# Optimization experiments

Measured on AMD Instinct MI355X. Metric: run time of the kernel, lower is better.

Reference implementation:

```python
import jax, jax.numpy as jnp
import numpy as np

B, M, D, DE = 2, 256, 256, 64  # batch, tokens, in_dim, dep_embed_dim


def setup_inputs() -> dict:
    key = jax.random.key(0)
    ks = jax.random.split(key, 10)
    features = jax.random.normal(ks[0], (B, M + 1, D), jnp.float32)
    dep_type_adj = jax.random.normal(ks[1], (B, M, M, DE), jnp.float32)
    adj = (jax.random.uniform(ks[2], (B, M, M)) < 0.05).astype(jnp.int32)
    idx = jnp.arange(M)
    adj = adj.at[:, idx, idx].set(1)
    asp_start = jax.random.randint(ks[3], (B,), 0, 200, dtype=jnp.int32)
    asp_end = asp_start + 16
    s = lambda fan_in: 1.0 / np.sqrt(fan_in)
    Wz = jax.random.normal(ks[4], (D, D), jnp.float32) * s(D)
    bz = jax.random.normal(ks[5], (D,), jnp.float32) * s(D)
    Wa = jax.random.normal(ks[6], (D + DE + D,), jnp.float32) * s(D + DE + D)
    Wm = jax.random.normal(ks[7], (D, D + DE), jnp.float32) * s(D + DE)
    Wh = jax.random.normal(ks[8], (D, 2 * D), jnp.float32) * s(2 * D)
    return dict(features=features, dep_type_adj=dep_type_adj, deprel_adj=adj,
                asp_start=asp_start, asp_end=asp_end,
                Wz=Wz, bz=bz, Wa=Wa, Wm=Wm, Wh=Wh)


def reference(features, dep_type_adj, deprel_adj, asp_start, asp_end, Wz, bz, Wa, Wm, Wh):
    # z_linear
    zf = features @ Wz.T + bz                              # [B, M+1, D]
    f = zf[:, 1:]                                          # token feats [B, M, D]
    asp = zf[0, 1:]                                        # NOTE: original indexes features[0] (batch 0)

    # candidate neighbors for node i: out-edges (i,j) then in-edges (j,i) -> 2M slots
    dep_cat = jnp.concatenate([dep_type_adj, jnp.swapaxes(dep_type_adj, 1, 2)], axis=2)  # [B,M,2M,DE]
    mask = jnp.concatenate([deprel_adj, jnp.swapaxes(deprel_adj, 1, 2)], axis=2) != 0    # [B,M,2M]

    # attention_layer weight split over [dep | neighbor_feat | aspect_feat]
    wa_dep, wa_nf, wa_asp = Wa[:DE], Wa[DE:DE + D], Wa[DE + D:]
    s = (jnp.einsum('bike,e->bik', dep_cat, wa_dep)
         + jnp.tile(f @ wa_nf, (1, 2))[:, None, :]
         + (asp @ wa_asp)[None, :, None])                  # [B,M,2M]
    s = jnp.where(s > 0, s, 0.01 * s)                      # LeakyReLU(0.01)
    big_neg = jnp.finfo(s.dtype).min
    w = jax.nn.softmax(jnp.where(mask, s, big_neg), axis=-1)
    w = jnp.where(mask, w, 0.0)                            # edge-softmax over valid neighbors

    # w_m over [dep | neighbor_feat]
    Wm_dep, Wm_f = Wm[:, :DE], Wm[:, DE:]
    nf_proj = jnp.tile(f @ Wm_f.T, (1, 2, 1))              # [B,2M,D], neighbor part (i-independent)
    msg = jax.nn.relu(jnp.einsum('bike,de->bikd', dep_cat, Wm_dep) + nf_proj[:, None])  # [B,M,2M,D]
    fused = jnp.einsum('bik,bikd->bid', w, msg)            # weighted aggregate [B,M,D]

    # w_h over [fused | aspect]
    out_asp = jax.nn.relu(fused @ Wh[:, :D].T + (asp @ Wh[:, D:].T)[None])  # [B,M,D]

    # only aspect-span nodes are updated; +1 offset into the token axis
    pos = jnp.arange(M)
    upd = (pos[None, :] >= asp_start[:, None]) & (pos[None, :] < asp_end[:, None])  # [B,M]
    tokens = jnp.where(upd[..., None], out_asp, features[:, 1:])
    return jnp.concatenate([features[:, :1], tokens], axis=1)  # dropout is identity at inference
```

## Files before the change

### kernel.cpp

```cpp
#include <hip/hip_runtime.h>
#include <hip/hip_bf16.h>
#include <cstdint>

#define BB 2
#define MM 256
#define DD 256
#define DE 64
#define K2 (2*MM)
#define WM_LD (DD+DE)
#define WH_LD (2*DD)
#define DEP_LD 68

__device__ float4 g_Wz4   [64*DD];
__device__ float4 g_Wm4   [64*DD];
__device__ float4 g_WmDep4[16*DD];
__device__ float4 g_Wh4lo [64*DD];
__device__ float4 g_Wh4hi [64*DD];
__device__ float g_fproj [BB*MM*DD];
__device__ float g_fnf   [BB*MM];
__device__ float g_aspdot[MM];
__device__ float g_asph  [MM*DD];

__global__ __launch_bounds__(256) void k_tr(const float* __restrict__ Wz,
                                            const float* __restrict__ Wm,
                                            const float* __restrict__ Wh,
                                            const float4* __restrict__ src,
                                            float4* __restrict__ dst, int n4) {
  const int t = threadIdx.x, blk = blockIdx.x;
  const int c = t & 63, r0 = t >> 6;
  __shared__ float tile[64][65];

  const int gidx = blk*256 + t;
  if (gidx < n4) dst[gidx] = src[gidx];

  const float* s = nullptr; float4* d4 = nullptr;
  int ld = 0, row0 = 0, col0 = 0, e4base = 0;
  if (blk < 16)      { s = Wz; ld = DD;    row0 = (blk>>2)*64; col0 = (blk&3)*64;      d4 = g_Wz4;    e4base = (blk&3)*16; }
  else if (blk < 32) { int x = blk-16; s = Wm; ld = WM_LD; row0 = (x>>2)*64; col0 = DE + (x&3)*64; d4 = g_Wm4; e4base = (x&3)*16; }
  else if (blk < 36) { int x = blk-32; s = Wm; ld = WM_LD; row0 = x*64;      col0 = 0;             d4 = g_WmDep4; e4base = 0; }
  else if (blk < 68) { int x = blk-36; int rt = x>>3, cg = x&7; s = Wh; ld = WH_LD; row0 = rt*64; col0 = cg*64;
                       d4 = (cg < 4) ? g_Wh4lo : g_Wh4hi; e4base = (cg&3)*16; }
  if (s) {
    #pragma unroll
    for (int rr = r0; rr < 64; rr += 4)
      tile[rr][c] = s[(size_t)(row0 + rr)*ld + col0 + c];
    __syncthreads();
    #pragma unroll
    for (int je = r0; je < 16; je += 4)
      d4[(size_t)(e4base + je)*DD + row0 + c] =
        make_float4(tile[c][4*je+0], tile[c][4*je+1], tile[c][4*je+2], tile[c][4*je+3]);
  }
}

__global__ __launch_bounds__(256) void k_pre(const float* __restrict__ feats,
                                             const float* __restrict__ bz,
                                             const float* __restrict__ Wa) {
  const int blk = blockIdx.x;
  const int b   = blk >> 7;
  const int m0  = (blk & 127) * 2;
  const int t   = threadIdx.x;

  __shared__ float fin[2][DD];
  __shared__ float fzsh[2][DD];

  fin[0][t] = feats[((size_t)b*(MM+1) + m0 + 1)*DD + t];
  fin[1][t] = feats[((size_t)b*(MM+1) + m0 + 2)*DD + t];
  __syncthreads();

  float a0 = 0.f, a1 = 0.f;
  #pragma unroll 8
  for (int e4 = 0; e4 < 64; ++e4) {
    const float4 w  = g_Wz4[(size_t)e4*DD + t];
    const float4 f0 = *(const float4*)&fin[0][e4*4];
    const float4 f1 = *(const float4*)&fin[1][e4*4];
    a0 += f0.x*w.x + f0.y*w.y + f0.z*w.z + f0.w*w.w;
    a1 += f1.x*w.x + f1.y*w.y + f1.z*w.z + f1.w*w.w;
  }
  const float bzt = bz[t];
  a0 += bzt; a1 += bzt;
  fzsh[0][t] = a0; fzsh[1][t] = a1;
  __syncthreads();

  const int wv = t >> 6, lane = t & 63;
  if (wv < 2) {
    float p = 0.f;
    for (int e = lane; e < DD; e += 64) p += fzsh[wv][e] * Wa[DE + e];
    for (int off = 32; off > 0; off >>= 1) p += __shfl_down(p, off, 64);
    if (lane == 0) g_fnf[b*MM + m0 + wv] = p;
  } else if (b == 0) {
    const int rr = wv - 2;
    float p = 0.f;
    for (int e = lane; e < DD; e += 64) p += fzsh[rr][e] * Wa[DE + DD + e];
    for (int off = 32; off > 0; off >>= 1) p += __shfl_down(p, off, 64);
    if (lane == 0) g_aspdot[m0 + rr] = p;
  }

  float p0 = 0.f, p1 = 0.f;
  #pragma unroll 8
  for (int e4 = 0; e4 < 64; ++e4) {
    const float4 w  = g_Wm4[(size_t)e4*DD + t];
    const float4 f0 = *(const float4*)&fzsh[0][e4*4];
    const float4 f1 = *(const float4*)&fzsh[1][e4*4];
    p0 += f0.x*w.x + f0.y*w.y + f0.z*w.z + f0.w*w.w;
    p1 += f1.x*w.x + f1.y*w.y + f1.z*w.z + f1.w*w.w;
  }
  g_fproj[((size_t)b*MM + m0    )*DD + t] = p0;
  g_fproj[((size_t)b*MM + m0 + 1)*DD + t] = p1;

  if (b == 0) {
    float q0 = 0.f, q1 = 0.f;
    #pragma unroll 8
    for (int e4 = 0; e4 < 64; ++e4) {
      const float4 w  = g_Wh4hi[(size_t)e4*DD + t];
      const float4 f0 = *(const float4*)&fzsh[0][e4*4];
      const float4 f1 = *(const float4*)&fzsh[1][e4*4];
      q0 += f0.x*w.x + f0.y*w.y + f0.z*w.z + f0.w*w.w;
      q1 += f1.x*w.x + f1.y*w.y + f1.z*w.z + f1.w*w.w;
    }
    g_asph[(size_t)(m0    )*DD + t] = q0;
    g_asph[(size_t)(m0 + 1)*DD + t] = q1;
  }
}

__global__ __launch_bounds__(256, 1) void k_attn(const float* __restrict__ dta,
                                                 const int*   __restrict__ adj,
                                                 const int*   __restrict__ a_start,
                                                 const int*   __restrict__ a_end,
                                                 const float* __restrict__ Wa,
                                                 float* __restrict__ out) {
  const int b = blockIdx.x >> 4;
  const int r = blockIdx.x & 15;
  const int i = a_start[b] + r;
  if (i >= a_end[b] || i >= MM) return;
  const int t = threadIdx.x;
  const int lane = t & 63, wv = t >> 6;
  const int d = t;

  __shared__ int   act[K2];
  __shared__ float sv [K2];
  __shared__ int   wcnt[8];
  __shared__ float wrm [4];
  __shared__ float wrs [4];
  __shared__ float wadep[DE];
  __shared__ float fnfsh[MM];
  __shared__ float depsh[64*DEP_LD];
  __shared__ float fproj_sh[64][DD];
  __shared__ float fused_sh[DD];

  const int mval0 = adj[((size_t)b*MM + i)*MM + t];
  const int mval1 = adj[((size_t)b*MM + t)*MM + i];
  float4 wm4[16];
  #pragma unroll
  for (int e4 = 0; e4 < 16; ++e4) wm4[e4] = g_WmDep4[(size_t)e4*DD + d];
  fnfsh[t] = g_fnf[b*MM + t];
  if (t < DE) wadep[t] = Wa[t];
  const float aspdot_i = g_aspdot[i];
  const float asph_i   = g_asph[(size_t)i*DD + d];

  const bool on0 = (mval0 != 0);
  const bool on1 = (mval1 != 0);
  const unsigned long long b0 = __ballot(on0);
  const unsigned long long b1 = __ballot(on1);
  if (lane == 0) { wcnt[wv] = __popcll(b0); wcnt[4+wv] = __popcll(b1); }
  __syncthreads();
  const int tot0 = wcnt[0] + wcnt[1] + wcnt[2] + wcnt[3];
  const int na   = tot0 + wcnt[4] + wcnt[5] + wcnt[6] + wcnt[7];
  {
    int off0 = 0, off1 = tot0;
    for (int w2 = 0; w2 < wv; ++w2) { off0 += wcnt[w2]; off1 += wcnt[4+w2]; }
    off0 += __popcll(b0 & ((1ull << lane) - 1ull));
    off1 += __popcll(b1 & ((1ull << lane) - 1ull));
    if (on0) act[off0] = t;
    if (on1) act[off1] = MM + t;
  }
  __syncthreads();

  const int jj = t >> 2, sub = t & 3;
  for (int base = 0; base < na; base += 64) {
    const int j = base + jj;
    float p = 0.f; int k = 0;
    if (j < na) {
      k = act[j];
      const float* dv = (k < MM) ? dta + (((size_t)b*MM + i)*MM + k)*DE
                                 : dta + (((size_t)b*MM + (k - MM))*MM + i)*DE;
      const float4* dv4 = (const float4*)dv + sub*4;
      const float4 v0 = dv4[0], v1 = dv4[1], v2 = dv4[2], v3 = dv4[3];
      const float* wa = wadep + sub*16;
      p = v0.x*wa[0]  + v0.y*wa[1]  + v0.z*wa[2]  + v0.w*wa[3]
        + v1.x*wa[4]  + v1.y*wa[5]  + v1.z*wa[6]  + v1.w*wa[7]
        + v2.x*wa[8]  + v2.y*wa[9]  + v2.z*wa[10] + v2.w*wa[11]
        + v3.x*wa[12] + v3.y*wa[13] + v3.z*wa[14] + v3.w*wa[15];
      if (base == 0) {
        float4* ds = (float4*)(depsh + jj*DEP_LD + sub*16);
        ds[0] = v0; ds[1] = v1; ds[2] = v2; ds[3] = v3;
      }
    }
    p += __shfl_xor(p, 1, 64);
    p += __shfl_xor(p, 2, 64);
    if (j < na && sub == 0) {
      const float s = p + fnfsh[k & (MM-1)] + aspdot_i;
      sv[j] = (s > 0.f) ? s : 0.01f * s;
    }
  }

  const int cnt0 = (na < 64) ? na : 64;
  const int nq0  = cnt0 * 64;
  float4 stash[16];
  #pragma unroll
  for (int rr = 0; rr < 16; ++rr) {
    const int q = t + rr*256;
    if (q < nq0) {
      const int jl = q >> 6, c4 = q & 63;
      const int k = act[jl];
      stash[rr] = *((const float4*)(g_fproj + ((size_t)b*MM + (k & (MM-1)))*DD) + c4);
    }
  }
  __syncthreads();

  {
    float part = -3.4e38f;
    for (int j = t; j < na; j += 256) part = fmaxf(part, sv[j]);
    for (int off = 32; off > 0; off >>= 1) part = fmaxf(part, __shfl_down(part, off, 64));
    if (lane == 0) wrm[wv] = part;
  }
  __syncthreads();
  const float mx = fmaxf(fmaxf(wrm[0], wrm[1]), fmaxf(wrm[2], wrm[3]));
  {
    float psum = 0.f;
    for (int j = t; j < na; j += 256) { float e = expf(sv[j] - mx); sv[j] = e; psum += e; }
    for (int off = 32; off > 0; off >>= 1) psum += __shfl_down(psum, off, 64);
    if (lane == 0) wrs[wv] = psum;
  }
  __syncthreads();
  const float inv = 1.f / (wrs[0] + wrs[1] + wrs[2] + wrs[3]);
  for (int j = t; j < na; j += 256) sv[j] *= inv;
  #pragma unroll
  for (int rr = 0; rr < 16; ++rr) {
    const int q = t + rr*256;
    if (q < nq0) { const int jl = q >> 6, c4 = q & 63; *(float4*)&fproj_sh[jl][c4*4] = stash[rr]; }
  }
  __syncthreads();

  float acc = 0.f;
  for (int base = 0; base < na; base += 64) {
    const int cnt = min(64, na - base);
    if (base > 0) {
      __syncthreads();
      for (int q = t; q < cnt*64; q += 256) {
        const int jl = q >> 6, c4 = q & 63;
        const int k = act[base + jl];
        *(float4*)&fproj_sh[jl][c4*4] =
          *((const float4*)(g_fproj + ((size_t)b*MM + (k & (MM-1)))*DD) + c4);
      }
      for (int q = t; q < cnt*16; q += 256) {
        const int jl = q >> 4, e4 = q & 15;
        const int k = act[base + jl];
        const float* dv = (k < MM) ? dta + (((size_t)b*MM + i)*MM + k)*DE
                                   : dta + (((size_t)b*MM + (k - MM))*MM + i)*DE;
        *(float4*)(depsh + jl*DEP_LD + e4*4) = ((const float4*)dv)[e4];
      }
      __syncthreads();
    }
    #pragma unroll 2
    for (int jl = 0; jl < cnt; ++jl) {
      const float4* dp = (const float4*)(depsh + jl*DEP_LD);
      float dot = 0.f;
      #pragma unroll
      for (int e4 = 0; e4 < 16; ++e4) {
        const float4 v = dp[e4];
        const float4 w = wm4[e4];
        dot += v.x*w.x + v.y*w.y + v.z*w.z + v.w*w.w;
      }
      float msg = dot + fproj_sh[jl][d];
      msg = (msg > 0.f) ? msg : 0.f;
      acc += sv[base + jl] * msg;
    }
  }
  fused_sh[d] = acc;
  __syncthreads();

  float o = asph_i;
  #pragma unroll 8
  for (int e4 = 0; e4 < 64; ++e4) {
    const float4 w = g_Wh4lo[(size_t)e4*DD + d];
    const float4 f = *(const float4*)&fused_sh[e4*4];
    o += f.x*w.x + f.y*w.y + f.z*w.z + f.w*w.w;
  }
  out[((size_t)b*(MM+1) + i + 1)*DD + d] = (o > 0.f) ? o : 0.f;
}

extern "C" void kernel_launch(void* const* d_in, const int* in_sizes, int n_in,
                              void* d_out, int out_size, void* d_ws, size_t ws_size,
                              hipStream_t stream) {
  const float* feats   = (const float*)d_in[0];
  const float* dta     = (const float*)d_in[1];
  const int*   adj     = (const int*)  d_in[2];
  const int*   a_start = (const int*)  d_in[3];
  const int*   a_end   = (const int*)  d_in[4];
  const float* Wz      = (const float*)d_in[5];
  const float* bz      = (const float*)d_in[6];
  const float* Wa      = (const float*)d_in[7];
  const float* Wm      = (const float*)d_in[8];
  const float* Wh      = (const float*)d_in[9];
  float* out = (float*)d_out;

  const int n4 = BB*(MM+1)*DD/4;
  k_tr  <<<132, 256, 0, stream>>>(Wz, Wm, Wh, (const float4*)feats, (float4*)out, n4);
  k_pre <<<BB*MM/2, 256, 0, stream>>>(feats, bz, Wa);
  k_attn<<<BB*16, 256, 0, stream>>>(dta, adj, a_start, a_end, Wa, out);
}
```

Baseline: 144.1 us.

## Skip unused aspect projections, rotate weight sweeps, hoist fproj stash loads

k_pre now computes the aspect dot product and the Wh-hi aspect projection only for rows inside either batch's aspect span, skipping most of that matvec work. The weight loops in k_pre and k_attn start at a block-dependent rotation so concurrent blocks touch different weight rows, meant to spread cache and channel contention. The fproj stash loads in k_attn are issued before the score loop so their latency overlaps it, and the message loop unroll goes from 2 to 4. The rotations add index arithmetic and the larger unroll may raise register pressure.

Result: slower. 155.7 us (+8.0%).

```diff
diff --git a/kernel.cpp b/kernel.cpp
--- a/kernel.cpp
+++ b/kernel.cpp
@@ -54,11 +54,14 @@
 
 __global__ __launch_bounds__(256) void k_pre(const float* __restrict__ feats,
                                              const float* __restrict__ bz,
-                                             const float* __restrict__ Wa) {
+                                             const float* __restrict__ Wa,
+                                             const int*   __restrict__ a_start,
+                                             const int*   __restrict__ a_end) {
   const int blk = blockIdx.x;
   const int b   = blk >> 7;
   const int m0  = (blk & 127) * 2;
   const int t   = threadIdx.x;
+  const int rot = blk & 63;
 
   __shared__ float fin[2][DD];
   __shared__ float fzsh[2][DD];
@@ -69,7 +72,8 @@
 
   float a0 = 0.f, a1 = 0.f;
   #pragma unroll 8
-  for (int e4 = 0; e4 < 64; ++e4) {
+  for (int it = 0; it < 64; ++it) {
+    const int e4 = (it + rot) & 63;
     const float4 w  = g_Wz4[(size_t)e4*DD + t];
     const float4 f0 = *(const float4*)&fin[0][e4*4];
     const float4 f1 = *(const float4*)&fin[1][e4*4];
@@ -77,11 +81,11 @@
     a1 += f1.x*w.x + f1.y*w.y + f1.z*w.z + f1.w*w.w;
   }
   const float bzt = bz[t];
-  a0 += bzt; a1 += bzt;
-  fzsh[0][t] = a0; fzsh[1][t] = a1;
+  fzsh[0][t] = a0 + bzt; fzsh[1][t] = a1 + bzt;
   __syncthreads();
 
   const int wv = t >> 6, lane = t & 63;
+  const int s0 = a_start[0], e0 = a_end[0], s1 = a_start[1], e1 = a_end[1];
   if (wv < 2) {
     float p = 0.f;
     for (int e = lane; e < DD; e += 64) p += fzsh[wv][e] * Wa[DE + e];
@@ -89,15 +93,19 @@
     if (lane == 0) g_fnf[b*MM + m0 + wv] = p;
   } else if (b == 0) {
     const int rr = wv - 2;
-    float p = 0.f;
-    for (int e = lane; e < DD; e += 64) p += fzsh[rr][e] * Wa[DE + DD + e];
-    for (int off = 32; off > 0; off >>= 1) p += __shfl_down(p, off, 64);
-    if (lane == 0) g_aspdot[m0 + rr] = p;
+    const int ri = m0 + rr;
+    if ((ri >= s0 && ri < e0) || (ri >= s1 && ri < e1)) {
+      float p = 0.f;
+      for (int e = lane; e < DD; e += 64) p += fzsh[rr][e] * Wa[DE + DD + e];
+      for (int off = 32; off > 0; off >>= 1) p += __shfl_down(p, off, 64);
+      if (lane == 0) g_aspdot[ri] = p;
+    }
   }
 
   float p0 = 0.f, p1 = 0.f;
   #pragma unroll 8
-  for (int e4 = 0; e4 < 64; ++e4) {
+  for (int it = 0; it < 64; ++it) {
+    const int e4 = (it + rot) & 63;
     const float4 w  = g_Wm4[(size_t)e4*DD + t];
     const float4 f0 = *(const float4*)&fzsh[0][e4*4];
     const float4 f1 = *(const float4*)&fzsh[1][e4*4];
@@ -108,17 +116,22 @@
   g_fproj[((size_t)b*MM + m0 + 1)*DD + t] = p1;
 
   if (b == 0) {
-    float q0 = 0.f, q1 = 0.f;
-    #pragma unroll 8
-    for (int e4 = 0; e4 < 64; ++e4) {
-      const float4 w  = g_Wh4hi[(size_t)e4*DD + t];
-      const float4 f0 = *(const float4*)&fzsh[0][e4*4];
-      const float4 f1 = *(const float4*)&fzsh[1][e4*4];
-      q0 += f0.x*w.x + f0.y*w.y + f0.z*w.z + f0.w*w.w;
-      q1 += f1.x*w.x + f1.y*w.y + f1.z*w.z + f1.w*w.w;
-    }
-    g_asph[(size_t)(m0    )*DD + t] = q0;
-    g_asph[(size_t)(m0 + 1)*DD + t] = q1;
+    const bool need0 = ((m0   >= s0 && m0   < e0) || (m0   >= s1 && m0   < e1));
+    const bool need1 = ((m0+1 >= s0 && m0+1 < e0) || (m0+1 >= s1 && m0+1 < e1));
+    if (need0 || need1) {
+      float q0 = 0.f, q1 = 0.f;
+      #pragma unroll 8
+      for (int it = 0; it < 64; ++it) {
+        const int e4 = (it + rot) & 63;
+        const float4 w  = g_Wh4hi[(size_t)e4*DD + t];
+        const float4 f0 = *(const float4*)&fzsh[0][e4*4];
+        const float4 f1 = *(const float4*)&fzsh[1][e4*4];
+        q0 += f0.x*w.x + f0.y*w.y + f0.z*w.z + f0.w*w.w;
+        q1 += f1.x*w.x + f1.y*w.y + f1.z*w.z + f1.w*w.w;
+      }
+      if (need0) g_asph[(size_t)(m0    )*DD + t] = q0;
+      if (need1) g_asph[(size_t)(m0 + 1)*DD + t] = q1;
+    }
   }
 }
 
@@ -135,6 +148,8 @@
   const int t = threadIdx.x;
   const int lane = t & 63, wv = t >> 6;
   const int d = t;
+  const int rot16 = blockIdx.x & 15;
+  const int rot64 = (blockIdx.x * 2) & 63;
 
   __shared__ int   act[K2];
   __shared__ float sv [K2];
@@ -151,7 +166,10 @@
   const int mval1 = adj[((size_t)b*MM + t)*MM + i];
   float4 wm4[16];
   #pragma unroll
-  for (int e4 = 0; e4 < 16; ++e4) wm4[e4] = g_WmDep4[(size_t)e4*DD + d];
+  for (int it = 0; it < 16; ++it) {
+    const int e4 = (it + rot16) & 15;
+    wm4[e4] = g_WmDep4[(size_t)e4*DD + d];
+  }
   fnfsh[t] = g_fnf[b*MM + t];
   if (t < DE) wadep[t] = Wa[t];
   const float aspdot_i = g_aspdot[i];
@@ -174,6 +192,19 @@
     if (on1) act[off1] = MM + t;
   }
   __syncthreads();
+
+  const int cnt0 = (na < 64) ? na : 64;
+  const int nq0  = cnt0 * 64;
+  float4 stash[16];
+  #pragma unroll
+  for (int rr = 0; rr < 16; ++rr) {
+    const int q = t + rr*256;
+    if (q < nq0) {
+      const int jl = q >> 6, c4 = q & 63;
+      const int k = act[jl];
+      stash[rr] = *((const float4*)(g_fproj + ((size_t)b*MM + (k & (MM-1)))*DD) + c4);
+    }
+  }
 
   const int jj = t >> 2, sub = t & 3;
   for (int base = 0; base < na; base += 64) {
@@ -202,19 +233,6 @@
       sv[j] = (s > 0.f) ? s : 0.01f * s;
     }
   }
-
-  const int cnt0 = (na < 64) ? na : 64;
-  const int nq0  = cnt0 * 64;
-  float4 stash[16];
-  #pragma unroll
-  for (int rr = 0; rr < 16; ++rr) {
-    const int q = t + rr*256;
-    if (q < nq0) {
-      const int jl = q >> 6, c4 = q & 63;
-      const int k = act[jl];
-      stash[rr] = *((const float4*)(g_fproj + ((size_t)b*MM + (k & (MM-1)))*DD) + c4);
-    }
-  }
   __syncthreads();
 
   {
@@ -261,7 +279,7 @@
       }
       __syncthreads();
     }
-    #pragma unroll 2
+    #pragma unroll 4
     for (int jl = 0; jl < cnt; ++jl) {
       const float4* dp = (const float4*)(depsh + jl*DEP_LD);
       float dot = 0.f;
@@ -281,7 +299,8 @@
 
   float o = asph_i;
   #pragma unroll 8
-  for (int e4 = 0; e4 < 64; ++e4) {
+  for (int it = 0; it < 64; ++it) {
+    const int e4 = (it + rot64) & 63;
     const float4 w = g_Wh4lo[(size_t)e4*DD + d];
     const float4 f = *(const float4*)&fused_sh[e4*4];
     o += f.x*w.x + f.y*w.y + f.z*w.z + f.w*w.w;
@@ -306,6 +325,6 @@
 
   const int n4 = BB*(MM+1)*DD/4;
   k_tr  <<<132, 256, 0, stream>>>(Wz, Wm, Wh, (const float4*)feats, (float4*)out, n4);
-  k_pre <<<BB*MM/2, 256, 0, stream>>>(feats, bz, Wa);
+  k_pre <<<BB*MM/2, 256, 0, stream>>>(feats, bz, Wa, a_start, a_end);
   k_attn<<<BB*16, 256, 0, stream>>>(dta, adj, a_start, a_end, Wa, out);
 }
```
